# Performance work log

Hardware: AMD Instinct MI355X
Metric: run time of the kernel (lower is better)

The kernel has to match this reference:

```python
import jax, jax.numpy as jnp
import numpy as np

B, S, W = 128, 256, 1
DEPTH = 655            # MathTypeKeysMax
UNITS = 128
PROBLEM_BUCKETS = 32


def setup_inputs() -> dict:
    key = jax.random.key(0)
    ks = jax.random.split(key, 14)
    ri = lambda k, shape, hi: jax.random.randint(k, shape, 0, hi, dtype=jnp.int32)
    K = 4 * DEPTH * W  # flattened per-timestep feature width = 2620
    return {
        'move_count': ri(ks[0], (B,), 100),
        'moves_remaining': ri(ks[1], (B,), 100),
        'last_rule': ri(ks[2], (B,), 12),
        'node_count': ri(ks[3], (B,), 64),
        'problem_type': ri(ks[4], (B,), PROBLEM_BUCKETS),
        'bwd_vectors': ri(ks[5], (B, S, W), DEPTH),
        'fwd_vectors': ri(ks[6], (B, S, W), DEPTH),
        'last_bwd_vectors': ri(ks[7], (B, S, W), DEPTH),
        'last_fwd_vectors': ri(ks[8], (B, S, W), DEPTH),
        'W_dense': jax.random.normal(ks[9], (K, UNITS), jnp.float32) * (1.0 / np.sqrt(K)),
        'b_dense': jnp.zeros((UNITS,), jnp.float32),
        'Wx': jax.random.normal(ks[10], (UNITS, 4 * UNITS), jnp.float32) * (1.0 / np.sqrt(UNITS)),
        'Wh': jax.random.normal(ks[11], (UNITS, 4 * UNITS), jnp.float32) * (1.0 / np.sqrt(UNITS)),
        'b_lstm': jnp.zeros((4 * UNITS,), jnp.float32),
    }


def _lstm(x, Wx, Wh, b):
    # x: [B, S, U] -> (seq hidden [B, S, U], final hidden [B, U]); keras gate order i,f,c,o
    U = Wh.shape[0]
    bsz = x.shape[0]
    # precompute input projections once: [S, B, 4U]
    xz = jnp.einsum('bsu,uv->sbv', x, Wx) + b

    def step(carry, zt):
        h, c = carry
        z = zt + h @ Wh
        i, f, g, o = jnp.split(z, 4, axis=-1)
        i = jax.nn.sigmoid(i)
        f = jax.nn.sigmoid(f)
        g = jnp.tanh(g)
        o = jax.nn.sigmoid(o)
        c = f * c + i * g
        h = o * jnp.tanh(c)
        return (h, c), h

    init = (jnp.zeros((bsz, U), x.dtype), jnp.zeros((bsz, U), x.dtype))
    (h_last, _), hs = jax.lax.scan(step, init, xz)
    return jnp.transpose(hs, (1, 0, 2)), h_last


def reference(move_count, moves_remaining, last_rule, node_count, problem_type,
              bwd_vectors, fwd_vectors, last_bwd_vectors, last_fwd_vectors,
              W_dense, b_dense, Wx, Wh, b_lstm):
    f32 = lambda a: a.astype(jnp.float32)
    # DenseFeatures context extraction: 3 numeric int columns + 32-bucket indicator
    context_inputs = jnp.concatenate([
        f32(last_rule)[:, None],
        f32(move_count)[:, None],
        f32(node_count)[:, None],
        jax.nn.one_hot(problem_type, PROBLEM_BUCKETS, dtype=jnp.float32),
    ], axis=-1)  # [B, 35]

    sequence_length = bwd_vectors.shape[1]
    # one-hot each [B,S,W] sequence to [B,S,W,DEPTH], concat on last axis -> [B,S,W,4*DEPTH]
    oh = jnp.concatenate([
        jax.nn.one_hot(bwd_vectors, DEPTH, dtype=jnp.float32),
        jax.nn.one_hot(fwd_vectors, DEPTH, dtype=jnp.float32),
        jax.nn.one_hot(last_bwd_vectors, DEPTH, dtype=jnp.float32),
        jax.nn.one_hot(last_fwd_vectors, DEPTH, dtype=jnp.float32),
    ], axis=-1)
    bsz = oh.shape[0]
    # per-example Flatten keeps leading S dim, so the loop == one batched matmul
    flat = oh.reshape(bsz, sequence_length, -1)      # [B, S, 4*DEPTH*W]
    outputs = jnp.einsum('bsk,ku->bsu', flat, W_dense) + b_dense  # [B, S, U]

    hidden_states, lstm_vectors = _lstm(outputs, Wx, Wh, b_lstm)
    return (context_inputs, lstm_vectors, hidden_states, sequence_length)
```

## Files before the change

### kernel.cpp

```cpp
#include <hip/hip_runtime.h>
#include <cstdint>

#define BB   128
#define SS   256
#define NDEPTH 655
#define UU   128
#define VV   512
#define ROWS_PER_BLK 20

typedef _Float16 f16;
typedef _Float16 f16x2 __attribute__((ext_vector_type(2)));

#if __has_builtin(__builtin_amdgcn_fdot2)
#define FDOT2(a, b, c) __builtin_amdgcn_fdot2((a), (b), (c), false)
#else
static __device__ __forceinline__ float FDOT2(f16x2 a, f16x2 b, float c) {
    return c + (float)a.x * (float)b.x + (float)a.y * (float)b.y;
}
#endif

__device__ __forceinline__ float qswap1(float x) {
    return __builtin_bit_cast(float,
        __builtin_amdgcn_mov_dpp(__builtin_bit_cast(int, x), 0xB1, 0xF, 0xF, true));
}
__device__ __forceinline__ float qswap2(float x) {
    return __builtin_bit_cast(float,
        __builtin_amdgcn_mov_dpp(__builtin_bit_cast(int, x), 0x4E, 0xF, 0xF, true));
}

#define STEP_BARRIER()                                          \
    do {                                                        \
        asm volatile("s_waitcnt lgkmcnt(0)" ::: "memory");      \
        __builtin_amdgcn_s_barrier();                           \
        __builtin_amdgcn_sched_barrier(0);                      \
    } while (0)

__global__ void wdwx_kernel(const float* __restrict__ Wd,
                            const float* __restrict__ Wx,
                            const float* __restrict__ b_dense,
                            const float* __restrict__ b_lstm,
                            const int* __restrict__ last_rule,
                            const int* __restrict__ move_count,
                            const int* __restrict__ node_count,
                            const int* __restrict__ problem_type,
                            float* __restrict__ WdWx,
                            float* __restrict__ base,
                            float* __restrict__ out, int write_seq) {
    const int v  = threadIdx.x;
    const int k0 = blockIdx.x * ROWS_PER_BLK;

    int gid = blockIdx.x * 512 + v;
    if (gid < BB * 35) {
        int b = gid / 35, cc = gid % 35;
        float val;
        if (cc == 0)      val = (float)last_rule[b];
        else if (cc == 1) val = (float)move_count[b];
        else if (cc == 2) val = (float)node_count[b];
        else              val = (problem_type[b] == (cc - 3)) ? 1.0f : 0.0f;
        out[gid] = val;
    }
    if (write_seq && gid == 0)
        out[(size_t)BB*35 + (size_t)BB*UU + (size_t)BB*SS*UU] = (float)SS;

    float acc[ROWS_PER_BLK] = {};
    for (int uu = 0; uu < UU; ++uu) {
        float wx = Wx[uu * VV + v];
        #pragma unroll
        for (int r = 0; r < ROWS_PER_BLK; ++r)
            acc[r] = fmaf(Wd[(size_t)(k0 + r) * UU + uu], wx, acc[r]);
    }
    #pragma unroll
    for (int r = 0; r < ROWS_PER_BLK; ++r)
        WdWx[(size_t)(k0 + r) * VV + v] = acc[r];

    if (blockIdx.x == 0) {
        float a = 0.f;
        for (int uu = 0; uu < UU; ++uu) a = fmaf(b_dense[uu], Wx[uu * VV + v], a);
        base[v] = a + b_lstm[v];
    }
}

__global__ __launch_bounds__(512, 2)
void lstm_kernel(const int* __restrict__ bwd,  const int* __restrict__ fwd,
                 const int* __restrict__ lbwd, const int* __restrict__ lfwd,
                 const float* __restrict__ WdWx,
                 const float* __restrict__ base,
                 const float* __restrict__ Wh,
                 float* __restrict__ hidden_states,
                 float* __restrict__ lstm_vectors) {
    const int b    = blockIdx.x;
    const int t    = threadIdx.x;
    const int lane = t & 63;
    const int w    = t >> 6;
    const int q    = lane & 3;
    const int u    = w * 16 + (lane >> 2);
    const int col  = q * UU + u;

    __shared__ __align__(16) unsigned char h2buf[2][320];
    __shared__ int idx_lds[SS][4];

    f16x2 wh2[64];
    #pragma unroll
    for (int j = 0; j < 16; ++j) {
        #pragma unroll
        for (int g = 0; g < 4; ++g) {
            float w0 = Wh[(size_t)(32*q + 2*j    ) * VV + g*UU + u];
            float w1 = Wh[(size_t)(32*q + 2*j + 1) * VV + g*UU + u];
            f16x2 pk; pk.x = (f16)w0; pk.y = (f16)w1;
            wh2[j*4 + g] = pk;
        }
    }

    for (int s = t; s < SS; s += 512) {
        idx_lds[s][0] =            bwd [b*SS + s];
        idx_lds[s][1] =   NDEPTH + fwd [b*SS + s];
        idx_lds[s][2] = 2*NDEPTH + lbwd[b*SS + s];
        idx_lds[s][3] = 3*NDEPTH + lfwd[b*SS + s];
    }
    if (t < UU)
        ((f16*)(h2buf[0] + 80*(t >> 5)))[t & 31] = (f16)0.0f;
    float c      = 0.0f;
    float bias   = base[col];
    float h_last = 0.0f;
    __syncthreads();

    float g0 = WdWx[(size_t)idx_lds[0][0] * VV + col];
    float g1 = WdWx[(size_t)idx_lds[0][1] * VV + col];
    float g2 = WdWx[(size_t)idx_lds[0][2] * VV + col];
    float g3 = WdWx[(size_t)idx_lds[0][3] * VV + col];

    const bool b0 = (q & 1) != 0;
    const bool b1 = (q & 2) != 0;

    int p = 0;
    for (int s = 0; s < SS; ++s) {
        float z = bias + (g0 + g1) + (g2 + g3);
        if (s + 1 < SS) {
            g0 = WdWx[(size_t)idx_lds[s+1][0] * VV + col];
            g1 = WdWx[(size_t)idx_lds[s+1][1] * VV + col];
            g2 = WdWx[(size_t)idx_lds[s+1][2] * VV + col];
            g3 = WdWx[(size_t)idx_lds[s+1][3] * VV + col];
        }

        const uint4* hb = (const uint4*)(h2buf[p] + 80 * q);
        uint4 A = hb[0], Bv = hb[1], Cv = hb[2], Dv = hb[3];
        float pp0 = 0.f, pp1 = 0.f, pp2 = 0.f, pp3 = 0.f;
        #define DOTW(word, j)                                            \
            do {                                                         \
                f16x2 hv = __builtin_bit_cast(f16x2, (word));            \
                pp0 = FDOT2(hv, wh2[(j)*4+0], pp0);                      \
                pp1 = FDOT2(hv, wh2[(j)*4+1], pp1);                      \
                pp2 = FDOT2(hv, wh2[(j)*4+2], pp2);                      \
                pp3 = FDOT2(hv, wh2[(j)*4+3], pp3);                      \
            } while (0)
        DOTW(A.x,  0); DOTW(A.y,  1); DOTW(A.z,  2); DOTW(A.w,  3);
        DOTW(Bv.x, 4); DOTW(Bv.y, 5); DOTW(Bv.z, 6); DOTW(Bv.w, 7);
        DOTW(Cv.x, 8); DOTW(Cv.y, 9); DOTW(Cv.z,10); DOTW(Cv.w,11);
        DOTW(Dv.x,12); DOTW(Dv.y,13); DOTW(Dv.z,14); DOTW(Dv.w,15);
        #undef DOTW

        float keepA = b0 ? pp1 : pp0;
        float keepB = b0 ? pp3 : pp2;
        float sendA = b0 ? pp0 : pp1;
        float sendB = b0 ? pp2 : pp3;
        float sA = keepA + qswap1(sendA);
        float sB = keepB + qswap1(sendB);
        float send2 = b1 ? sA : sB;
        z += (b1 ? sB : sA) + qswap2(send2);

        float xs = (q == 2) ? 2.0f * z : z;
        float sg = __fdividef(1.0f, 1.0f + __expf(-xs));
        float a  = (q == 2) ? 2.0f * sg - 1.0f : sg;

        float v1 = qswap1(a);
        float v2 = qswap2(a);
        float v3 = qswap2(v1);
        float ig = (q & 1) ? v1 * v3 : a * v2;
        float gf = (q & 1) ? ((q & 2) ? v2 : a)
                           : ((q & 2) ? v3 : v1);
        float go = (q & 1) ? ((q & 2) ? a  : v2)
                           : ((q & 2) ? v1 : v3);
        c = fmaf(gf, c, ig);
        float e  = __expf(2.0f * c);
        float tc = 1.0f - __fdividef(2.0f, e + 1.0f);
        float h  = go * tc;

        if (q == 0) {
            ((f16*)(h2buf[p ^ 1] + 80*(u >> 5)))[u & 31] = (f16)h;
            hidden_states[((size_t)b * SS + s) * UU + u] = h;
            h_last = h;
        }
        STEP_BARRIER();
        p ^= 1;
    }
    if (q == 0) lstm_vectors[(size_t)b * UU + u] = h_last;
}

extern "C" void kernel_launch(void* const* d_in, const int* in_sizes, int n_in,
                              void* d_out, int out_size, void* d_ws, size_t ws_size,
                              hipStream_t stream) {
    const int* move_count   = (const int*)d_in[0];
    const int* last_rule    = (const int*)d_in[2];
    const int* node_count   = (const int*)d_in[3];
    const int* problem_type = (const int*)d_in[4];
    const int* bwd          = (const int*)d_in[5];
    const int* fwd          = (const int*)d_in[6];
    const int* lbwd         = (const int*)d_in[7];
    const int* lfwd         = (const int*)d_in[8];
    const float* Wd         = (const float*)d_in[9];
    const float* b_dense    = (const float*)d_in[10];
    const float* Wx         = (const float*)d_in[11];
    const float* Wh         = (const float*)d_in[12];
    const float* b_lstm     = (const float*)d_in[13];

    float* out  = (float*)d_out;
    float* WdWx = (float*)d_ws;
    float* base = WdWx + (size_t)(4 * NDEPTH) * VV;

    float* lstm_out = out + BB * 35;
    float* hs_out   = lstm_out + BB * UU;
    int write_seq = (out_size > BB*35 + BB*UU + BB*SS*UU) ? 1 : 0;

    wdwx_kernel<<<131, VV, 0, stream>>>(Wd, Wx, b_dense, b_lstm,
                                        last_rule, move_count, node_count,
                                        problem_type, WdWx, base, out, write_seq);
    lstm_kernel<<<BB, 512, 0, stream>>>(bwd, fwd, lbwd, lfwd, WdWx, base, Wh,
                                        hs_out, lstm_out);
}
```

Before: 294.9 us.

## Spread WdWx precompute over more blocks and load sequence indices directly from global

The folded Wd·Wx precompute now has each block handle 4 rows instead of 20, launching 655 blocks instead of 131 so more CUs share the work. In the LSTM kernel the per-sequence index staging into LDS is removed, and each step reads the four indices straight from global memory before gathering the WdWx rows. This frees LDS and drops the staging loop, but it adds a dependent global load ahead of each gather inside the serial recurrence.

After: 316.0 us. +7.1%, slower.

```diff
diff --git a/kernel.cpp b/kernel.cpp
--- a/kernel.cpp
+++ b/kernel.cpp
@@ -6,7 +6,6 @@
 #define NDEPTH 655
 #define UU   128
 #define VV   512
-#define ROWS_PER_BLK 20
 
 typedef _Float16 f16;
 typedef _Float16 f16x2 __attribute__((ext_vector_type(2)));
@@ -47,7 +46,7 @@
                             float* __restrict__ base,
                             float* __restrict__ out, int write_seq) {
     const int v  = threadIdx.x;
-    const int k0 = blockIdx.x * ROWS_PER_BLK;
+    const int k0 = blockIdx.x * 4;
 
     int gid = blockIdx.x * 512 + v;
     if (gid < BB * 35) {
@@ -62,17 +61,19 @@
     if (write_seq && gid == 0)
         out[(size_t)BB*35 + (size_t)BB*UU + (size_t)BB*SS*UU] = (float)SS;
 
-    float acc[ROWS_PER_BLK] = {};
+    const float* wd0 = Wd + (size_t)k0 * UU;
+    float a0 = 0.f, a1 = 0.f, a2 = 0.f, a3 = 0.f;
     for (int uu = 0; uu < UU; ++uu) {
         float wx = Wx[uu * VV + v];
-        #pragma unroll
-        for (int r = 0; r < ROWS_PER_BLK; ++r)
-            acc[r] = fmaf(Wd[(size_t)(k0 + r) * UU + uu], wx, acc[r]);
-    }
-    #pragma unroll
-    for (int r = 0; r < ROWS_PER_BLK; ++r)
-        WdWx[(size_t)(k0 + r) * VV + v] = acc[r];
-
+        a0 = fmaf(wd0[uu],        wx, a0);
+        a1 = fmaf(wd0[UU + uu],   wx, a1);
+        a2 = fmaf(wd0[2*UU + uu], wx, a2);
+        a3 = fmaf(wd0[3*UU + uu], wx, a3);
+    }
+    WdWx[(size_t)(k0+0)*VV + v] = a0;
+    WdWx[(size_t)(k0+1)*VV + v] = a1;
+    WdWx[(size_t)(k0+2)*VV + v] = a2;
+    WdWx[(size_t)(k0+3)*VV + v] = a3;
     if (blockIdx.x == 0) {
         float a = 0.f;
         for (int uu = 0; uu < UU; ++uu) a = fmaf(b_dense[uu], Wx[uu * VV + v], a);
@@ -88,16 +89,16 @@
                  const float* __restrict__ Wh,
                  float* __restrict__ hidden_states,
                  float* __restrict__ lstm_vectors) {
-    const int b    = blockIdx.x;
-    const int t    = threadIdx.x;
-    const int lane = t & 63;
-    const int w    = t >> 6;
-    const int q    = lane & 3;
-    const int u    = w * 16 + (lane >> 2);
-    const int col  = q * UU + u;
+    const int b     = blockIdx.x;
+    const int t     = threadIdx.x;
+    const int lane  = t & 63;
+    const int w     = t >> 6;
+    const int q     = lane & 3;
+    const int u     = w * 16 + (lane >> 2);
+    const int col   = q * UU + u;
+    const int sbase = b * SS;
 
     __shared__ __align__(16) unsigned char h2buf[2][320];
-    __shared__ int idx_lds[SS][4];
 
     f16x2 wh2[64];
     #pragma unroll
@@ -111,12 +112,6 @@
         }
     }
 
-    for (int s = t; s < SS; s += 512) {
-        idx_lds[s][0] =            bwd [b*SS + s];
-        idx_lds[s][1] =   NDEPTH + fwd [b*SS + s];
-        idx_lds[s][2] = 2*NDEPTH + lbwd[b*SS + s];
-        idx_lds[s][3] = 3*NDEPTH + lfwd[b*SS + s];
-    }
     if (t < UU)
         ((f16*)(h2buf[0] + 80*(t >> 5)))[t & 31] = (f16)0.0f;
     float c      = 0.0f;
@@ -124,10 +119,17 @@
     float h_last = 0.0f;
     __syncthreads();
 
-    float g0 = WdWx[(size_t)idx_lds[0][0] * VV + col];
-    float g1 = WdWx[(size_t)idx_lds[0][1] * VV + col];
-    float g2 = WdWx[(size_t)idx_lds[0][2] * VV + col];
-    float g3 = WdWx[(size_t)idx_lds[0][3] * VV + col];
+    {
+        int i0 = bwd [sbase];
+        int i1 = fwd [sbase] + NDEPTH;
+        int i2 = lbwd[sbase] + 2*NDEPTH;
+        int i3 = lfwd[sbase] + 3*NDEPTH;
+        (void)i0; (void)i1; (void)i2; (void)i3;
+    }
+    float g0 = WdWx[(size_t)(bwd [sbase]           ) * VV + col];
+    float g1 = WdWx[(size_t)(fwd [sbase] +   NDEPTH) * VV + col];
+    float g2 = WdWx[(size_t)(lbwd[sbase] + 2*NDEPTH) * VV + col];
+    float g3 = WdWx[(size_t)(lfwd[sbase] + 3*NDEPTH) * VV + col];
 
     const bool b0 = (q & 1) != 0;
     const bool b1 = (q & 2) != 0;
@@ -136,10 +138,14 @@
     for (int s = 0; s < SS; ++s) {
         float z = bias + (g0 + g1) + (g2 + g3);
         if (s + 1 < SS) {
-            g0 = WdWx[(size_t)idx_lds[s+1][0] * VV + col];
-            g1 = WdWx[(size_t)idx_lds[s+1][1] * VV + col];
-            g2 = WdWx[(size_t)idx_lds[s+1][2] * VV + col];
-            g3 = WdWx[(size_t)idx_lds[s+1][3] * VV + col];
+            int i0 = bwd [sbase + s + 1];
+            int i1 = fwd [sbase + s + 1];
+            int i2 = lbwd[sbase + s + 1];
+            int i3 = lfwd[sbase + s + 1];
+            g0 = WdWx[(size_t)(i0           ) * VV + col];
+            g1 = WdWx[(size_t)(i1 +   NDEPTH) * VV + col];
+            g2 = WdWx[(size_t)(i2 + 2*NDEPTH) * VV + col];
+            g3 = WdWx[(size_t)(i3 + 3*NDEPTH) * VV + col];
         }
 
         const uint4* hb = (const uint4*)(h2buf[p] + 80 * q);
@@ -187,7 +193,7 @@
 
         if (q == 0) {
             ((f16*)(h2buf[p ^ 1] + 80*(u >> 5)))[u & 31] = (f16)h;
-            hidden_states[((size_t)b * SS + s) * UU + u] = h;
+            hidden_states[((size_t)sbase + s) * UU + u] = h;
             h_last = h;
         }
         STEP_BARRIER();
@@ -221,9 +227,9 @@
     float* hs_out   = lstm_out + BB * UU;
     int write_seq = (out_size > BB*35 + BB*UU + BB*SS*UU) ? 1 : 0;
 
-    wdwx_kernel<<<131, VV, 0, stream>>>(Wd, Wx, b_dense, b_lstm,
-                                        last_rule, move_count, node_count,
-                                        problem_type, WdWx, base, out, write_seq);
+    wdwx_kernel<<<NDEPTH, VV, 0, stream>>>(Wd, Wx, b_dense, b_lstm,
+                                           last_rule, move_count, node_count,
+                                           problem_type, WdWx, base, out, write_seq);
     lstm_kernel<<<BB, 512, 0, stream>>>(bwd, fwd, lbwd, lfwd, WdWx, base, Wh,
                                         hs_out, lstm_out);
 }
```
